# Kernel optimization log

Hardware: AMD Instinct MI355X
Metric: run time of the kernel (lower is better)

## Reference

```python
import jax, jax.numpy as jnp
import numpy as np

B, N, H = 32, 512, 128
LN_EPS = 1e-5

def _layernorm(x):
    # LayerNorm over last dim, no affine (elementwise_affine=False)
    mu = jnp.mean(x, axis=-1, keepdims=True)
    var = jnp.var(x, axis=-1, keepdims=True)
    return (x - mu) * jax.lax.rsqrt(var + LN_EPS)

def setup_inputs() -> dict:
    key = jax.random.key(0)
    k0, k1, k2, k3 = jax.random.split(key, 4)
    s = jax.random.normal(k0, (B, N, H), dtype=jnp.float32)
    ev = jax.random.normal(k1, (B, N, N, 3), dtype=jnp.float32)
    mask = (jax.random.uniform(k2, (B, N, N, 1)) > 0.5).astype(jnp.float32)
    W1 = jax.random.normal(k3, (H, H), dtype=jnp.float32) / np.sqrt(H)
    b1 = jnp.zeros((H,), dtype=jnp.float32)
    return {"s": s, "ev": ev, "mask": mask, "W1": W1, "b1": b1}

def reference(s, ev, mask, W1, b1):
    # lin1: Linear -> LayerNorm (no affine) -> SiLU
    h = jnp.einsum('bnh,kh->bnk', s, W1) + b1          # (B, N, H)
    h = jax.nn.silu(_layernorm(h))
    # Fused CFConv: v[b,i,c,d] = sum_j mask[b,i,j] * ev[b,i,j,c] * h[b,j,d]
    mev = ev * mask                                     # (B, N, N, 3)
    v = jnp.einsum('bijc,bjd->bicd', mev, h)            # (B, N, 3, H)
    return v
```

## Files before the change

### kernel.cpp

```cpp
#include <hip/hip_runtime.h>
#include <hip/hip_bf16.h>

#define B_ 32
#define N_ 512
#define H_ 128

typedef float f32x4 __attribute__((ext_vector_type(4)));
typedef short short8 __attribute__((ext_vector_type(8)));
typedef short short4v __attribute__((ext_vector_type(4)));

static __device__ __forceinline__ float bf2f(unsigned short u) {
  union { unsigned int ui; float f; } x;
  x.ui = ((unsigned int)u) << 16;
  return x.f;
}
static __device__ __forceinline__ unsigned short f2bf(float f) {
  __hip_bfloat16 h = __float2bfloat16(f);
  return *reinterpret_cast<unsigned short*>(&h);
}

__global__ __launch_bounds__(256) void lin_ln_silu_kernel(
    const float* __restrict__ s, const float* __restrict__ W1,
    const float* __restrict__ b1, unsigned short* __restrict__ h_t) {
  __shared__ float s_sh[32 * 132];
  __shared__ unsigned short w_sh[128 * 132];
  __shared__ unsigned short ht_sh[128 * 40];
  const int t = threadIdx.x;
  const int b = blockIdx.y;
  const int n0 = blockIdx.x * 32;

#pragma unroll
  for (int r = 0; r < 16; ++r) {
    int q = t + 256 * r;
    int d = q >> 5, part = q & 31;
    float4 v = *reinterpret_cast<const float4*>(W1 + d * H_ + part * 4);
    short4v w;
    w.x = (short)f2bf(v.x); w.y = (short)f2bf(v.y);
    w.z = (short)f2bf(v.z); w.w = (short)f2bf(v.w);
    *reinterpret_cast<short4v*>(&w_sh[d * 132 + part * 4]) = w;
  }
#pragma unroll
  for (int r = 0; r < 4; ++r) {
    int q = t + 256 * r;
    int n = q >> 5, part = q & 31;
    float4 v = *reinterpret_cast<const float4*>(
        s + ((size_t)b * N_ + n0 + n) * H_ + part * 4);
    *reinterpret_cast<float4*>(&s_sh[n * 132 + part * 4]) = v;
  }
  __syncthreads();

  const int a = t & 15;
  const int g = t >> 4;
  float acc[2][8];
#pragma unroll
  for (int nn = 0; nn < 2; ++nn)
#pragma unroll
    for (int dd = 0; dd < 8; ++dd) acc[nn][dd] = 0.f;

  float bias[8];
#pragma unroll
  for (int dd = 0; dd < 8; ++dd) bias[dd] = b1[dd * 16 + a];

  for (int k = 0; k < 128; k += 4) {
    float wf[8][4];
#pragma unroll
    for (int dd = 0; dd < 8; ++dd) {
      short4v wv =
          *reinterpret_cast<const short4v*>(&w_sh[(dd * 16 + a) * 132 + k]);
      wf[dd][0] = bf2f((unsigned short)wv.x);
      wf[dd][1] = bf2f((unsigned short)wv.y);
      wf[dd][2] = bf2f((unsigned short)wv.z);
      wf[dd][3] = bf2f((unsigned short)wv.w);
    }
#pragma unroll
    for (int nn = 0; nn < 2; ++nn) {
      float4 sv =
          *reinterpret_cast<const float4*>(&s_sh[(nn * 16 + g) * 132 + k]);
#pragma unroll
      for (int dd = 0; dd < 8; ++dd) {
        acc[nn][dd] += sv.x * wf[dd][0] + sv.y * wf[dd][1] +
                       sv.z * wf[dd][2] + sv.w * wf[dd][3];
      }
    }
  }

#pragma unroll
  for (int nn = 0; nn < 2; ++nn) {
    float s1 = 0.f, s2 = 0.f;
#pragma unroll
    for (int dd = 0; dd < 8; ++dd) {
      float x = acc[nn][dd] + bias[dd];
      acc[nn][dd] = x;
      s1 += x;
      s2 += x * x;
    }
#pragma unroll
    for (int off = 8; off >= 1; off >>= 1) {
      s1 += __shfl_xor(s1, off);
      s2 += __shfl_xor(s2, off);
    }
    float mean = s1 * (1.f / 128.f);
    float var = s2 * (1.f / 128.f) - mean * mean;
    float rs = rsqrtf(var + 1e-5f);
#pragma unroll
    for (int dd = 0; dd < 8; ++dd) {
      float x = (acc[nn][dd] - mean) * rs;
      float y = x / (1.f + __expf(-x));
      ht_sh[(dd * 16 + a) * 40 + nn * 16 + g] = f2bf(y);
    }
  }
  __syncthreads();

#pragma unroll
  for (int r = 0; r < 2; ++r) {
    int q = t + 256 * r;
    int d = q >> 2, part = q & 3;
    float4 v = *reinterpret_cast<const float4*>(&ht_sh[d * 40 + part * 8]);
    *reinterpret_cast<float4*>(
        h_t + ((size_t)b * 128 + d) * 512 + n0 + part * 8) = v;
  }
}

__global__ __launch_bounds__(256) void cfconv_mfma_kernel(
    const float* __restrict__ ev, const float* __restrict__ mask,
    const unsigned short* __restrict__ h_t, float* __restrict__ out) {
  __shared__ unsigned short ph[48 * 72];
  __shared__ unsigned short hh[128 * 72];
  const int t = threadIdx.x;
  const int b = blockIdx.y;
  const int i0 = blockIdx.x * 16;
  const int lane = t & 63;
  const int w = t >> 6;
  const int l15 = lane & 15;
  const int quad = lane >> 4;

  f32x4 acc[3][2];
#pragma unroll
  for (int mt = 0; mt < 3; ++mt)
#pragma unroll
    for (int nt = 0; nt < 2; ++nt)
#pragma unroll
      for (int e = 0; e < 4; ++e) acc[mt][nt][e] = 0.f;

  for (int j0 = 0; j0 < N_; j0 += 64) {
    __syncthreads();

#pragma unroll
    for (int r = 0; r < 4; ++r) {
      int q = t + 256 * r;
      int d = q >> 3, p8 = q & 7;
      float4 v = *reinterpret_cast<const float4*>(
          h_t + ((size_t)b * 128 + d) * 512 + j0 + p8 * 8);
      *reinterpret_cast<float4*>(&hh[d * 72 + p8 * 8]) = v;
    }

#pragma unroll
    for (int r = 0; r < 3; ++r) {
      int q = t + 256 * r;
      int i = q / 48, part = q % 48;
      int f0 = part * 4;
      const float* evbase =
          ev + ((size_t)((b * N_ + i0 + i)) * N_ + j0) * 3;
      float4 e4 = *reinterpret_cast<const float4*>(evbase + f0);
      const float* mrow = mask + (size_t)(b * N_ + i0 + i) * N_ + j0;
      int jlo = f0 / 3, jhi = (f0 + 3) / 3;
      float mlo = mrow[jlo], mhi = mrow[jhi];
      float evv[4] = {e4.x, e4.y, e4.z, e4.w};
#pragma unroll
      for (int e = 0; e < 4; ++e) {
        int f = f0 + e;
        int j = f / 3, c = f - 3 * j;
        float m = (j == jlo) ? mlo : mhi;
        ph[(c * 16 + i) * 72 + j] = f2bf(evv[e] * m);
      }
    }
    __syncthreads();

#pragma unroll
    for (int ks = 0; ks < 2; ++ks) {
      short8 av[3], bv[2];
#pragma unroll
      for (int mt = 0; mt < 3; ++mt)
        av[mt] = *reinterpret_cast<const short8*>(
            &ph[(mt * 16 + l15) * 72 + ks * 32 + quad * 8]);
#pragma unroll
      for (int nt = 0; nt < 2; ++nt) {
        int d = w * 32 + nt * 16 + l15;
        bv[nt] = *reinterpret_cast<const short8*>(
            &hh[d * 72 + ks * 32 + quad * 8]);
      }
#pragma unroll
      for (int mt = 0; mt < 3; ++mt)
#pragma unroll
        for (int nt = 0; nt < 2; ++nt)
          acc[mt][nt] = __builtin_amdgcn_mfma_f32_16x16x32_bf16(
              av[mt], bv[nt], acc[mt][nt], 0, 0, 0);
    }
  }

#pragma unroll
  for (int mt = 0; mt < 3; ++mt) {
#pragma unroll
    for (int nt = 0; nt < 2; ++nt) {
      int d = w * 32 + nt * 16 + l15;
#pragma unroll
      for (int r = 0; r < 4; ++r) {
        int i = i0 + quad * 4 + r;
        out[(((size_t)b * N_ + i) * 3 + mt) * H_ + d] = acc[mt][nt][r];
      }
    }
  }
}

extern "C" void kernel_launch(void* const* d_in, const int* in_sizes, int n_in,
                              void* d_out, int out_size, void* d_ws,
                              size_t ws_size, hipStream_t stream) {
  const float* s = (const float*)d_in[0];
  const float* ev = (const float*)d_in[1];
  const float* mask = (const float*)d_in[2];
  const float* W1 = (const float*)d_in[3];
  const float* b1 = (const float*)d_in[4];
  float* out = (float*)d_out;
  unsigned short* h_t = (unsigned short*)d_ws;

  lin_ln_silu_kernel<<<dim3(N_ / 32, B_), 256, 0, stream>>>(s, W1, b1, h_t);
  cfconv_mfma_kernel<<<dim3(N_ / 16, B_), 256, 0, stream>>>(ev, mask, h_t, out);
}
```

Before: 212.2 us.

## Prefetch next ev/mask/h tiles into registers and vectorize ev packing

The CFConv kernel now loads the next j-tile of h, ev and mask into registers right after the second barrier, so those global loads overlap with the MFMA work on the current tile. The ev/mask staging is also remapped so each thread handles 4 consecutive j values with three float4 ev loads and one float4 mask load, writing packed short4 vectors to LDS instead of scattered per-element stores with divisions. Barriers become raw s_barrier calls that wait only on LDS counters. The cost is higher register pressure from holding the prefetched tiles.

```diff
diff --git a/kernel.cpp b/kernel.cpp
--- a/kernel.cpp
+++ b/kernel.cpp
@@ -134,6 +134,12 @@
   const int l15 = lane & 15;
   const int quad = lane >> 4;
 
+  const int si = t >> 4;
+  const int sj = t & 15;
+  const float* evbase =
+      ev + ((size_t)(b * N_ + i0 + si)) * N_ * 3 + (size_t)sj * 12;
+  const float* mbase = mask + ((size_t)(b * N_ + i0 + si)) * N_ + sj * 4;
+
   f32x4 acc[3][2];
 #pragma unroll
   for (int mt = 0; mt < 3; ++mt)
@@ -142,39 +148,65 @@
 #pragma unroll
       for (int e = 0; e < 4; ++e) acc[mt][nt][e] = 0.f;
 
-  for (int j0 = 0; j0 < N_; j0 += 64) {
-    __syncthreads();
-
-#pragma unroll
-    for (int r = 0; r < 4; ++r) {
-      int q = t + 256 * r;
+  float4 hv[4];
+  float4 evv[3];
+  float4 mkv;
+
+#pragma unroll
+  for (int r2 = 0; r2 < 4; ++r2) {
+    int q = t + 256 * r2;
+    int d = q >> 3, p8 = q & 7;
+    hv[r2] = *reinterpret_cast<const float4*>(
+        h_t + ((size_t)b * 128 + d) * 512 + p8 * 8);
+  }
+#pragma unroll
+  for (int e = 0; e < 3; ++e)
+    evv[e] = *reinterpret_cast<const float4*>(evbase + e * 4);
+  mkv = *reinterpret_cast<const float4*>(mbase);
+
+  for (int r = 0; r < 8; ++r) {
+    asm volatile("s_waitcnt lgkmcnt(0)" ::: "memory");
+    __builtin_amdgcn_s_barrier();
+
+#pragma unroll
+    for (int r2 = 0; r2 < 4; ++r2) {
+      int q = t + 256 * r2;
       int d = q >> 3, p8 = q & 7;
-      float4 v = *reinterpret_cast<const float4*>(
-          h_t + ((size_t)b * 128 + d) * 512 + j0 + p8 * 8);
-      *reinterpret_cast<float4*>(&hh[d * 72 + p8 * 8]) = v;
-    }
-
-#pragma unroll
-    for (int r = 0; r < 3; ++r) {
-      int q = t + 256 * r;
-      int i = q / 48, part = q % 48;
-      int f0 = part * 4;
-      const float* evbase =
-          ev + ((size_t)((b * N_ + i0 + i)) * N_ + j0) * 3;
-      float4 e4 = *reinterpret_cast<const float4*>(evbase + f0);
-      const float* mrow = mask + (size_t)(b * N_ + i0 + i) * N_ + j0;
-      int jlo = f0 / 3, jhi = (f0 + 3) / 3;
-      float mlo = mrow[jlo], mhi = mrow[jhi];
-      float evv[4] = {e4.x, e4.y, e4.z, e4.w};
-#pragma unroll
-      for (int e = 0; e < 4; ++e) {
-        int f = f0 + e;
-        int j = f / 3, c = f - 3 * j;
-        float m = (j == jlo) ? mlo : mhi;
-        ph[(c * 16 + i) * 72 + j] = f2bf(evv[e] * m);
-      }
-    }
-    __syncthreads();
+      *reinterpret_cast<float4*>(&hh[d * 72 + p8 * 8]) = hv[r2];
+    }
+    {
+      float f[12] = {evv[0].x, evv[0].y, evv[0].z, evv[0].w,
+                     evv[1].x, evv[1].y, evv[1].z, evv[1].w,
+                     evv[2].x, evv[2].y, evv[2].z, evv[2].w};
+      float mk[4] = {mkv.x, mkv.y, mkv.z, mkv.w};
+#pragma unroll
+      for (int c = 0; c < 3; ++c) {
+        short4v pk;
+        pk.x = (short)f2bf(f[0 * 3 + c] * mk[0]);
+        pk.y = (short)f2bf(f[1 * 3 + c] * mk[1]);
+        pk.z = (short)f2bf(f[2 * 3 + c] * mk[2]);
+        pk.w = (short)f2bf(f[3 * 3 + c] * mk[3]);
+        *reinterpret_cast<short4v*>(&ph[(c * 16 + si) * 72 + sj * 4]) = pk;
+      }
+    }
+
+    asm volatile("s_waitcnt lgkmcnt(0)" ::: "memory");
+    __builtin_amdgcn_s_barrier();
+
+    if (r < 7) {
+      const int jn = (r + 1) * 64;
+#pragma unroll
+      for (int r2 = 0; r2 < 4; ++r2) {
+        int q = t + 256 * r2;
+        int d = q >> 3, p8 = q & 7;
+        hv[r2] = *reinterpret_cast<const float4*>(
+            h_t + ((size_t)b * 128 + d) * 512 + jn + p8 * 8);
+      }
+#pragma unroll
+      for (int e = 0; e < 3; ++e)
+        evv[e] = *reinterpret_cast<const float4*>(evbase + (size_t)jn * 3 + e * 4);
+      mkv = *reinterpret_cast<const float4*>(mbase + jn);
+    }
 
 #pragma unroll
     for (int ks = 0; ks < 2; ++ks) {
```

New measurement: 228.8 us. +7.8%, slower.

## Software-pipeline global loads two tiles ahead in cfconv kernel with vectorized staging

Applied to the files above, without the earlier changes.

Restructures the cfconv main loop so global loads of h, ev and mask for the next two j-tiles are issued into registers before the current tile is computed, using double register buffers. Loads are also reorganized so each thread reads contiguous float4 chunks of ev and mask and writes packed short4 to LDS instead of scalar per-element stores with divisions. Barriers wait only on LDS counters so global loads can stay in flight across them, and launch bounds request 4 blocks per CU. The cost is higher register pressure from the two buffers, which may limit occupancy.

```diff
diff --git a/kernel.cpp b/kernel.cpp
--- a/kernel.cpp
+++ b/kernel.cpp
@@ -121,7 +121,7 @@
   }
 }
 
-__global__ __launch_bounds__(256) void cfconv_mfma_kernel(
+__global__ __launch_bounds__(256, 4) void cfconv_mfma_kernel(
     const float* __restrict__ ev, const float* __restrict__ mask,
     const unsigned short* __restrict__ h_t, float* __restrict__ out) {
   __shared__ unsigned short ph[48 * 72];
@@ -134,6 +134,15 @@
   const int l15 = lane & 15;
   const int quad = lane >> 4;
 
+  const int si = t >> 4;
+  const int sj = t & 15;
+  const int hd = t >> 3;
+  const int hp = t & 7;
+  const float* evbase =
+      ev + ((size_t)(b * N_ + i0 + si)) * N_ * 3 + (size_t)sj * 12;
+  const float* mbase = mask + ((size_t)(b * N_ + i0 + si)) * N_ + sj * 4;
+  const unsigned short* hbase = h_t + (size_t)b * 128 * 512;
+
   f32x4 acc[3][2];
 #pragma unroll
   for (int mt = 0; mt < 3; ++mt)
@@ -142,61 +151,91 @@
 #pragma unroll
       for (int e = 0; e < 4; ++e) acc[mt][nt][e] = 0.f;
 
-  for (int j0 = 0; j0 < N_; j0 += 64) {
-    __syncthreads();
-
-#pragma unroll
-    for (int r = 0; r < 4; ++r) {
-      int q = t + 256 * r;
-      int d = q >> 3, p8 = q & 7;
-      float4 v = *reinterpret_cast<const float4*>(
-          h_t + ((size_t)b * 128 + d) * 512 + j0 + p8 * 8);
-      *reinterpret_cast<float4*>(&hh[d * 72 + p8 * 8]) = v;
-    }
-
-#pragma unroll
-    for (int r = 0; r < 3; ++r) {
-      int q = t + 256 * r;
-      int i = q / 48, part = q % 48;
-      int f0 = part * 4;
-      const float* evbase =
-          ev + ((size_t)((b * N_ + i0 + i)) * N_ + j0) * 3;
-      float4 e4 = *reinterpret_cast<const float4*>(evbase + f0);
-      const float* mrow = mask + (size_t)(b * N_ + i0 + i) * N_ + j0;
-      int jlo = f0 / 3, jhi = (f0 + 3) / 3;
-      float mlo = mrow[jlo], mhi = mrow[jhi];
-      float evv[4] = {e4.x, e4.y, e4.z, e4.w};
-#pragma unroll
-      for (int e = 0; e < 4; ++e) {
-        int f = f0 + e;
-        int j = f / 3, c = f - 3 * j;
-        float m = (j == jlo) ? mlo : mhi;
-        ph[(c * 16 + i) * 72 + j] = f2bf(evv[e] * m);
-      }
-    }
-    __syncthreads();
-
-#pragma unroll
-    for (int ks = 0; ks < 2; ++ks) {
-      short8 av[3], bv[2];
-#pragma unroll
-      for (int mt = 0; mt < 3; ++mt)
-        av[mt] = *reinterpret_cast<const short8*>(
-            &ph[(mt * 16 + l15) * 72 + ks * 32 + quad * 8]);
-#pragma unroll
-      for (int nt = 0; nt < 2; ++nt) {
-        int d = w * 32 + nt * 16 + l15;
-        bv[nt] = *reinterpret_cast<const short8*>(
-            &hh[d * 72 + ks * 32 + quad * 8]);
-      }
-#pragma unroll
-      for (int mt = 0; mt < 3; ++mt)
-#pragma unroll
-        for (int nt = 0; nt < 2; ++nt)
-          acc[mt][nt] = __builtin_amdgcn_mfma_f32_16x16x32_bf16(
-              av[mt], bv[nt], acc[mt][nt], 0, 0, 0);
-    }
-  }
+  float4 hvA[4], evvA[3], mkvA;
+  float4 hvB[4], evvB[3], mkvB;
+
+#define ISSUE(HV, EVV, MKV, JR)                                              \
+  do {                                                                       \
+    const int jn_ = (JR)*64;                                                 \
+    _Pragma("unroll") for (int r2 = 0; r2 < 4; ++r2) {                       \
+      int d_ = hd + 32 * r2;                                                 \
+      HV[r2] = *reinterpret_cast<const float4*>(                             \
+          hbase + (size_t)d_ * 512 + jn_ + hp * 8);                          \
+    }                                                                        \
+    _Pragma("unroll") for (int e_ = 0; e_ < 3; ++e_) {                       \
+      EVV[e_] = *reinterpret_cast<const float4*>(evbase + (size_t)jn_ * 3 +  \
+                                                 e_ * 4);                    \
+    }                                                                        \
+    MKV = *reinterpret_cast<const float4*>(mbase + jn_);                     \
+  } while (0)
+
+#define STAGE(HV, EVV, MKV)                                                  \
+  do {                                                                       \
+    _Pragma("unroll") for (int r2 = 0; r2 < 4; ++r2) {                       \
+      int d_ = hd + 32 * r2;                                                 \
+      *reinterpret_cast<float4*>(&hh[d_ * 72 + hp * 8]) = HV[r2];            \
+    }                                                                        \
+    float f_[12] = {EVV[0].x, EVV[0].y, EVV[0].z, EVV[0].w,                  \
+                    EVV[1].x, EVV[1].y, EVV[1].z, EVV[1].w,                  \
+                    EVV[2].x, EVV[2].y, EVV[2].z, EVV[2].w};                 \
+    float mk_[4] = {MKV.x, MKV.y, MKV.z, MKV.w};                             \
+    _Pragma("unroll") for (int c_ = 0; c_ < 3; ++c_) {                       \
+      short4v pk_;                                                           \
+      pk_.x = (short)f2bf(f_[0 * 3 + c_] * mk_[0]);                          \
+      pk_.y = (short)f2bf(f_[1 * 3 + c_] * mk_[1]);                          \
+      pk_.z = (short)f2bf(f_[2 * 3 + c_] * mk_[2]);                          \
+      pk_.w = (short)f2bf(f_[3 * 3 + c_] * mk_[3]);                          \
+      *reinterpret_cast<short4v*>(&ph[(c_ * 16 + si) * 72 + sj * 4]) = pk_;  \
+    }                                                                        \
+  } while (0)
+
+#define COMPUTE()                                                            \
+  do {                                                                       \
+    _Pragma("unroll") for (int ks = 0; ks < 2; ++ks) {                       \
+      short8 av[3], bv[2];                                                   \
+      _Pragma("unroll") for (int mt = 0; mt < 3; ++mt) av[mt] =              \
+          *reinterpret_cast<const short8*>(                                  \
+              &ph[(mt * 16 + l15) * 72 + ks * 32 + quad * 8]);               \
+      _Pragma("unroll") for (int nt = 0; nt < 2; ++nt) {                     \
+        int d_ = w * 32 + nt * 16 + l15;                                     \
+        bv[nt] = *reinterpret_cast<const short8*>(                           \
+            &hh[d_ * 72 + ks * 32 + quad * 8]);                              \
+      }                                                                      \
+      _Pragma("unroll") for (int mt = 0; mt < 3; ++mt)                       \
+          _Pragma("unroll") for (int nt = 0; nt < 2; ++nt) acc[mt][nt] =     \
+          __builtin_amdgcn_mfma_f32_16x16x32_bf16(av[mt], bv[nt],            \
+                                                  acc[mt][nt], 0, 0, 0);     \
+    }                                                                        \
+  } while (0)
+
+#define SYNC_LGKM()                                   \
+  do {                                                \
+    asm volatile("s_waitcnt lgkmcnt(0)" ::: "memory"); \
+    __builtin_amdgcn_s_barrier();                     \
+  } while (0)
+
+  ISSUE(hvA, evvA, mkvA, 0);
+  ISSUE(hvB, evvB, mkvB, 1);
+
+#pragma unroll
+  for (int rr = 0; rr < 4; ++rr) {
+    SYNC_LGKM();
+    STAGE(hvA, evvA, mkvA);
+    SYNC_LGKM();
+    if (rr < 3) ISSUE(hvA, evvA, mkvA, 2 * rr + 2);
+    COMPUTE();
+
+    SYNC_LGKM();
+    STAGE(hvB, evvB, mkvB);
+    SYNC_LGKM();
+    if (rr < 3) ISSUE(hvB, evvB, mkvB, 2 * rr + 3);
+    COMPUTE();
+  }
+
+#undef ISSUE
+#undef STAGE
+#undef COMPUTE
+#undef SYNC_LGKM
 
 #pragma unroll
   for (int mt = 0; mt < 3; ++mt) {
```

After: 212.1 us. No clear change (-0.1%).

## Double-buffer cfconv tiles with direct global-to-LDS loads and manual waitcnt pipeline

Applied to the files above, without the earlier changes.

Rewrites the cfconv main loop as a two-stage software pipeline. Raw ev and h_t tiles are loaded straight into double-buffered LDS with global_load_lds, and the mask is prefetched into registers with inline asm. The mask multiply and bf16 conversion then run from LDS while the next tile is in flight, h tiles use an XOR-swizzled layout to avoid bank conflicts, and the launch bound asks for 2 blocks per CU. The goal is to hide the global load latency of the memory-bound ev stream. The cost is more LDS, hand-tuned vmcnt counts and barriers that are fragile to get right, and a fully unrolled loop.

```diff
diff --git a/kernel.cpp b/kernel.cpp
--- a/kernel.cpp
+++ b/kernel.cpp
@@ -17,6 +17,12 @@
 static __device__ __forceinline__ unsigned short f2bf(float f) {
   __hip_bfloat16 h = __float2bfloat16(f);
   return *reinterpret_cast<unsigned short*>(&h);
+}
+
+static __device__ __forceinline__ void gld16(const void* g, void* l) {
+  __builtin_amdgcn_global_load_lds(
+      (const __attribute__((address_space(1))) unsigned int*)g,
+      (__attribute__((address_space(3))) unsigned int*)l, 16, 0, 0);
 }
 
 __global__ __launch_bounds__(256) void lin_ln_silu_kernel(
@@ -121,18 +127,35 @@
   }
 }
 
-__global__ __launch_bounds__(256) void cfconv_mfma_kernel(
+__global__ __launch_bounds__(256, 2) void cfconv_mfma_kernel(
     const float* __restrict__ ev, const float* __restrict__ mask,
     const unsigned short* __restrict__ h_t, float* __restrict__ out) {
+  __shared__ float evr[2][3072];
+  __shared__ unsigned short hhs[2][8192];
   __shared__ unsigned short ph[48 * 72];
-  __shared__ unsigned short hh[128 * 72];
   const int t = threadIdx.x;
   const int b = blockIdx.y;
   const int i0 = blockIdx.x * 16;
-  const int lane = t & 63;
-  const int w = t >> 6;
-  const int l15 = lane & 15;
-  const int quad = lane >> 4;
+  const int w = t >> 6, l = t & 63;
+  const int l15 = l & 15, quad = l >> 4;
+  const int si = t >> 4, sj = t & 15;
+  const int xr = (l15 & 7) << 3;
+
+  const char* evB = (const char*)ev + ((size_t)(b * N_) + i0) * (N_ * 12);
+  int ev_row[3], ev_off[3];
+#pragma unroll
+  for (int e = 0; e < 3; ++e) {
+    int L = (w * 3 + e) * 64 + l;
+    ev_row[e] = L / 48;
+    ev_off[e] = (L - ev_row[e] * 48) * 16;
+  }
+  const char* hhB = (const char*)h_t + (size_t)b * (128 * 512 * 2);
+  int hh_go[4];
+#pragma unroll
+  for (int r2 = 0; r2 < 4; ++r2)
+    hh_go[r2] = ((r2 * 32 + w * 8 + (l >> 3)) << 10) +
+                ((((l & 7) ^ (l >> 3))) << 4);
+  const float* mB = mask + ((size_t)(b * N_) + i0 + si) * N_ + sj * 4;
 
   f32x4 acc[3][2];
 #pragma unroll
@@ -142,61 +165,116 @@
 #pragma unroll
       for (int e = 0; e < 4; ++e) acc[mt][nt][e] = 0.f;
 
-  for (int j0 = 0; j0 < N_; j0 += 64) {
-    __syncthreads();
-
-#pragma unroll
-    for (int r = 0; r < 4; ++r) {
-      int q = t + 256 * r;
-      int d = q >> 3, p8 = q & 7;
-      float4 v = *reinterpret_cast<const float4*>(
-          h_t + ((size_t)b * 128 + d) * 512 + j0 + p8 * 8);
-      *reinterpret_cast<float4*>(&hh[d * 72 + p8 * 8]) = v;
-    }
-
-#pragma unroll
-    for (int r = 0; r < 3; ++r) {
-      int q = t + 256 * r;
-      int i = q / 48, part = q % 48;
-      int f0 = part * 4;
-      const float* evbase =
-          ev + ((size_t)((b * N_ + i0 + i)) * N_ + j0) * 3;
-      float4 e4 = *reinterpret_cast<const float4*>(evbase + f0);
-      const float* mrow = mask + (size_t)(b * N_ + i0 + i) * N_ + j0;
-      int jlo = f0 / 3, jhi = (f0 + 3) / 3;
-      float mlo = mrow[jlo], mhi = mrow[jhi];
-      float evv[4] = {e4.x, e4.y, e4.z, e4.w};
-#pragma unroll
-      for (int e = 0; e < 4; ++e) {
-        int f = f0 + e;
-        int j = f / 3, c = f - 3 * j;
-        float m = (j == jlo) ? mlo : mhi;
-        ph[(c * 16 + i) * 72 + j] = f2bf(evv[e] * m);
-      }
-    }
-    __syncthreads();
-
-#pragma unroll
-    for (int ks = 0; ks < 2; ++ks) {
-      short8 av[3], bv[2];
-#pragma unroll
-      for (int mt = 0; mt < 3; ++mt)
-        av[mt] = *reinterpret_cast<const short8*>(
-            &ph[(mt * 16 + l15) * 72 + ks * 32 + quad * 8]);
-#pragma unroll
-      for (int nt = 0; nt < 2; ++nt) {
-        int d = w * 32 + nt * 16 + l15;
-        bv[nt] = *reinterpret_cast<const short8*>(
-            &hh[d * 72 + ks * 32 + quad * 8]);
-      }
-#pragma unroll
-      for (int mt = 0; mt < 3; ++mt)
-#pragma unroll
-        for (int nt = 0; nt < 2; ++nt)
-          acc[mt][nt] = __builtin_amdgcn_mfma_f32_16x16x32_bf16(
-              av[mt], bv[nt], acc[mt][nt], 0, 0, 0);
-    }
-  }
+  f32x4 mkA, mkB;
+
+#define SB() __builtin_amdgcn_sched_barrier(0)
+#define ALOAD4(DST, PTR) \
+  asm volatile("global_load_dwordx4 %0, %1, off" : "=v"(DST) : "v"(PTR))
+
+#define ISSUE_TILE(Q, JR)                                              \
+  do {                                                                 \
+    _Pragma("unroll") for (int e_ = 0; e_ < 3; ++e_)                   \
+        gld16(evB + (size_t)ev_row[e_] * 6144 + (JR)*768 + ev_off[e_], \
+              (char*)&evr[Q][0] + (w * 3 + e_) * 1024);                \
+    _Pragma("unroll") for (int r2_ = 0; r2_ < 4; ++r2_)                \
+        gld16(hhB + hh_go[r2_] + (JR)*128,                             \
+              (char*)&hhs[Q][0] + (r2_ * 32 + w * 8) * 128);           \
+  } while (0)
+
+#define ISSUE_MASK(MK, JR)                 \
+  do {                                     \
+    const float* pm_ = mB + (JR)*64;       \
+    ALOAD4(MK, pm_);                       \
+  } while (0)
+
+#define CONVERT(P, MK)                                                   \
+  do {                                                                   \
+    const float* ep_ = &evr[P][si * 192 + sj * 12];                      \
+    f32x4 e0_ = *reinterpret_cast<const f32x4*>(ep_);                    \
+    f32x4 e1_ = *reinterpret_cast<const f32x4*>(ep_ + 4);                \
+    f32x4 e2_ = *reinterpret_cast<const f32x4*>(ep_ + 8);                \
+    float f_[12] = {e0_[0], e0_[1], e0_[2], e0_[3], e1_[0], e1_[1],      \
+                    e1_[2], e1_[3], e2_[0], e2_[1], e2_[2], e2_[3]};     \
+    float mk_[4] = {MK[0], MK[1], MK[2], MK[3]};                         \
+    _Pragma("unroll") for (int c_ = 0; c_ < 3; ++c_) {                   \
+      short4v pk_;                                                       \
+      pk_.x = (short)f2bf(f_[0 * 3 + c_] * mk_[0]);                      \
+      pk_.y = (short)f2bf(f_[1 * 3 + c_] * mk_[1]);                      \
+      pk_.z = (short)f2bf(f_[2 * 3 + c_] * mk_[2]);                      \
+      pk_.w = (short)f2bf(f_[3 * 3 + c_] * mk_[3]);                      \
+      *reinterpret_cast<short4v*>(&ph[(c_ * 16 + si) * 72 + sj * 4]) =   \
+          pk_;                                                           \
+    }                                                                    \
+  } while (0)
+
+#define COMPUTE(P)                                                        \
+  do {                                                                    \
+    _Pragma("unroll") for (int ks = 0; ks < 2; ++ks) {                    \
+      short8 av[3], bv[2];                                                \
+      _Pragma("unroll") for (int mt = 0; mt < 3; ++mt) av[mt] =           \
+          *reinterpret_cast<const short8*>(                               \
+              &ph[(mt * 16 + l15) * 72 + ks * 32 + quad * 8]);            \
+      _Pragma("unroll") for (int nt = 0; nt < 2; ++nt) {                  \
+        int d_ = w * 32 + nt * 16 + l15;                                  \
+        bv[nt] = *reinterpret_cast<const short8*>(                        \
+            &hhs[P][d_ * 64 + ((ks * 32 + quad * 8) ^ xr)]);              \
+      }                                                                   \
+      _Pragma("unroll") for (int mt = 0; mt < 3; ++mt)                    \
+          _Pragma("unroll") for (int nt = 0; nt < 2; ++nt) acc[mt][nt] =  \
+          __builtin_amdgcn_mfma_f32_16x16x32_bf16(av[mt], bv[nt],         \
+                                                  acc[mt][nt], 0, 0, 0);  \
+    }                                                                     \
+  } while (0)
+
+#define ROUND7(P, Q, MKC, MKN, JN)            \
+  do {                                        \
+    SB(); __builtin_amdgcn_s_barrier(); SB(); \
+    ISSUE_TILE(Q, JN);                        \
+    SB();                                     \
+    asm volatile("s_waitcnt vmcnt(7)");       \
+    SB();                                     \
+    __builtin_amdgcn_s_barrier(); SB();       \
+    CONVERT(P, MKC);                          \
+    ISSUE_MASK(MKN, JN);                      \
+    SB();                                     \
+    asm volatile("s_waitcnt lgkmcnt(0)");     \
+    __builtin_amdgcn_s_barrier(); SB();       \
+    COMPUTE(P);                               \
+  } while (0)
+
+#define ROUND_LAST(P, MKC)                    \
+  do {                                        \
+    SB(); __builtin_amdgcn_s_barrier(); SB(); \
+    asm volatile("s_waitcnt vmcnt(0)");       \
+    SB();                                     \
+    __builtin_amdgcn_s_barrier(); SB();       \
+    CONVERT(P, MKC);                          \
+    SB();                                     \
+    asm volatile("s_waitcnt lgkmcnt(0)");     \
+    __builtin_amdgcn_s_barrier(); SB();       \
+    COMPUTE(P);                               \
+  } while (0)
+
+  ISSUE_TILE(0, 0);
+  ISSUE_MASK(mkA, 0);
+
+  ROUND7(0, 1, mkA, mkB, 1);
+  ROUND7(1, 0, mkB, mkA, 2);
+  ROUND7(0, 1, mkA, mkB, 3);
+  ROUND7(1, 0, mkB, mkA, 4);
+  ROUND7(0, 1, mkA, mkB, 5);
+  ROUND7(1, 0, mkB, mkA, 6);
+  ROUND7(0, 1, mkA, mkB, 7);
+  ROUND_LAST(1, mkB);
+
+#undef ROUND_LAST
+#undef ROUND7
+#undef COMPUTE
+#undef CONVERT
+#undef ISSUE_MASK
+#undef ISSUE_TILE
+#undef ALOAD4
+#undef SB
 
 #pragma unroll
   for (int mt = 0; mt < 3; ++mt) {
```

After: 206.5 us. 1.03x faster.
